# Kernel tuning notes

Hardware: AMD Instinct MI355X
Metric: run time of the kernel (lower is better)

Reference implementation:

```python
import jax, jax.numpy as jnp
import numpy as np
from jax import lax

# Dims: mel, reduction factor, encoder dim, prenet hidden, attention dim,
# attention-RNN units, decoder-RNN units, location-conv filters/kernel.
MEL, R, ENC, PRE, ATTN, ARNN, DRNN, FILT, K = 80, 2, 512, 256, 128, 1024, 1024, 32, 31
B, T_ENC, T_DEC = 64, 200, 400


def setup_inputs() -> dict:
    key = jax.random.key(0)
    ks = jax.random.split(key, 16)
    g = lambda i, shape: jax.random.normal(ks[i], shape, jnp.float32) * 0.02
    return {
        "encoder_outputs": jax.random.normal(ks[0], (B, T_ENC, ENC), jnp.float32),
        "inputs": jax.random.normal(ks[1], (B, T_DEC, MEL), jnp.float32),
        # prenet
        "W_pre1": g(2, (PRE, MEL)), "b_pre1": jnp.zeros((PRE,), jnp.float32),
        "W_pre2": g(3, (PRE, PRE)), "b_pre2": jnp.zeros((PRE,), jnp.float32),
        # memory layer (no bias)
        "W_mem": g(4, (ATTN, ENC)),
        # attention LSTMCell: input = prenet(256) + context(512)
        "Wih_a": g(5, (4 * ARNN, PRE + ENC)), "Whh_a": g(6, (4 * ARNN, ARNN)),
        "bih_a": jnp.zeros((4 * ARNN,), jnp.float32), "bhh_a": jnp.zeros((4 * ARNN,), jnp.float32),
        # location-sensitive attention
        "W_q": g(7, (ATTN, ARNN)),
        "W_conv": g(8, (FILT, 1, K)),
        "W_loc": g(9, (ATTN, FILT)),
        "v": g(10, (ATTN,)),
        # decoder LSTMCell: input = attn_rnn_h(1024) + context(512)
        "Wih_d": g(11, (4 * DRNN, ARNN + ENC)), "Whh_d": g(12, (4 * DRNN, DRNN)),
        "bih_d": jnp.zeros((4 * DRNN,), jnp.float32), "bhh_d": jnp.zeros((4 * DRNN,), jnp.float32),
        # output projections from cat(decoder_h, context) = 1536
        "W_mel": g(13, (MEL * R, DRNN + ENC)), "b_mel": jnp.zeros((MEL * R,), jnp.float32),
        "W_stop": g(14, (1, DRNN + ENC)), "b_stop": jnp.zeros((1,), jnp.float32),
    }


def _lstm(x, h, c, Wih, Whh, bih, bhh):
    # torch LSTMCell gate order: i, f, g, o
    gates = x @ Wih.T + bih + h @ Whh.T + bhh
    i, f, gg, o = jnp.split(gates, 4, axis=-1)
    c2 = jax.nn.sigmoid(f) * c + jax.nn.sigmoid(i) * jnp.tanh(gg)
    return jax.nn.sigmoid(o) * jnp.tanh(c2), c2


def _forward(encoder_outputs, inputs, W_pre1, b_pre1, W_pre2, b_pre2, W_mem,
             Wih_a, Whh_a, bih_a, bhh_a, W_q, W_conv, W_loc, v,
             Wih_d, Whh_d, bih_d, bhh_d, W_mel, b_mel, W_stop, b_stop):
    b, t_enc, _ = encoder_outputs.shape
    steps = inputs.shape[1] // R
    pm = encoder_outputs @ W_mem.T  # (B, T_enc, ATTN) processed memory
    # teacher-forced inputs: step 0 uses zeros, step k uses inputs[:, k*R-1]
    tf = inputs[:, R - 1::R, :][:, :steps - 1, :]
    dec_in = jnp.concatenate([jnp.zeros((b, 1, MEL), inputs.dtype), tf], axis=1).transpose(1, 0, 2)
    pad = (K - 1) // 2

    def step(carry, x):
        ah, ac, dh, dc, ctx, aw = carry
        # prenet (dropout disabled / eval mode)
        p = jax.nn.relu(jax.nn.relu(x @ W_pre1.T + b_pre1) @ W_pre2.T + b_pre2)
        ah, ac = _lstm(jnp.concatenate([p, ctx], -1), ah, ac, Wih_a, Whh_a, bih_a, bhh_a)
        # location feature from previous alignment: conv1d over time
        loc = lax.conv_general_dilated(aw[:, None, :], W_conv, (1,), [(pad, pad)],
                                       dimension_numbers=("NCH", "OIH", "NCH"))  # (B, FILT, T_enc)
        feat = jnp.tanh((ah @ W_q.T)[:, None, :] + jnp.einsum("bft,af->bta", loc, W_loc) + pm)
        align = jax.nn.softmax(jnp.einsum("bta,a->bt", feat, v), axis=-1)  # (B, T_enc)
        ctx = jnp.einsum("bt,btd->bd", align, encoder_outputs)  # (B, ENC)
        dh, dc = _lstm(jnp.concatenate([ah, ctx], -1), dh, dc, Wih_d, Whh_d, bih_d, bhh_d)
        proj = jnp.concatenate([dh, ctx], -1)  # (B, DRNN+ENC)
        mel = (proj @ W_mel.T + b_mel).reshape(b, R, MEL)
        stop = jax.nn.sigmoid(proj @ W_stop.T + b_stop)[:, 0]
        return (ah, ac, dh, dc, ctx, align), (mel, stop, align)

    z = lambda d: jnp.zeros((b, d), encoder_outputs.dtype)
    carry0 = (z(ARNN), z(ARNN), z(DRNN), z(DRNN), z(ENC),
              jnp.zeros((b, t_enc), encoder_outputs.dtype))
    _, (mels, stops, aligns) = lax.scan(step, carry0, dec_in)
    mel_outputs = mels.transpose(1, 0, 2, 3).reshape(b, steps * R, MEL)  # (B, T_dec, MEL)
    stop_tokens = jnp.repeat(stops.transpose(1, 0), R, axis=1)  # (B, T_dec)
    attn_scores = aligns.transpose(1, 0, 2)  # (B, steps, T_enc)
    return mel_outputs, stop_tokens, attn_scores


def reference(encoder_outputs, inputs, W_pre1, b_pre1, W_pre2, b_pre2, W_mem,
              Wih_a, Whh_a, bih_a, bhh_a, W_q, W_conv, W_loc, v,
              Wih_d, Whh_d, bih_d, bhh_d, W_mel, b_mel, W_stop, b_stop):
    return _forward(encoder_outputs, inputs, W_pre1, b_pre1, W_pre2, b_pre2, W_mem,
                    Wih_a, Whh_a, bih_a, bhh_a, W_q, W_conv, W_loc, v,
                    Wih_d, Whh_d, bih_d, bhh_d, W_mel, b_mel, W_stop, b_stop)
```

## Files before the change

### kernel.cpp

```cpp
#include <hip/hip_runtime.h>
#include <hip/hip_bf16.h>
#include <stdint.h>

#define STEPS  200
#define KA     1792
#define KD     2560
#define SLOT   (64*2560)

using bf16 = __bf16;
typedef __bf16 bf16x8 __attribute__((ext_vector_type(8)));
typedef float  f32x4  __attribute__((ext_vector_type(4)));
typedef unsigned int       u32;
typedef unsigned long long u64;

union U2h { u32 u; bf16 h[2]; };

#define MFMA16(a,b,c) __builtin_amdgcn_mfma_f32_16x16x32_bf16((a),(b),(c),0,0,0)

__device__ __forceinline__ float sigf(float x){ return 1.f/(1.f+__expf(-x)); }
__device__ __forceinline__ float tanhf_(float x){
  float ax = fabsf(x);
  float e  = __expf(-2.f*ax);
  float t  = (1.f-e)/(1.f+e);
  return x < 0.f ? -t : t;
}

__global__ void cvt_kernel(const float* __restrict__ s, bf16* __restrict__ d, int n){
  int i = blockIdx.x*256 + threadIdx.x;
  if (i < n) d[i] = (bf16)s[i];
}
__global__ void cvt_pad_kernel(const float* __restrict__ s, bf16* __restrict__ d,
                               int rows, int cin, int cout){
  int i = blockIdx.x*256 + threadIdx.x;
  if (i >= rows*cout) return;
  int r = i / cout, c = i % cout;
  d[i] = (bf16)(c < cin ? s[(size_t)r*cin + c] : 0.f);
}
__global__ void build_wa_pack(const float* __restrict__ Wiha, const float* __restrict__ Whha,
                              bf16* __restrict__ d){
  int i = blockIdx.x*256 + threadIdx.x;
  if (i >= 4096*1792) return;
  int r = i / 1792, k = i % 1792;
  int q2 = r >> 4, g = (r >> 2) & 3, j = r & 3;
  int orig = g*1024 + q2*4 + j;
  float v = (k < 768) ? Wiha[(size_t)orig*768 + k] : Whha[(size_t)orig*1024 + (k - 768)];
  d[i] = (bf16)v;
}
__global__ void build_wd_pack(const float* __restrict__ Wihd, const float* __restrict__ Whhd,
                              bf16* __restrict__ d){
  int i = blockIdx.x*256 + threadIdx.x;
  if (i >= 4096*2560) return;
  int r = i / 2560, k = i % 2560;
  int q2 = r >> 4, g = (r >> 2) & 3, j = r & 3;
  int orig = g*1024 + q2*4 + j;
  float v;
  if (k < 512)        v = Wihd[(size_t)orig*1536 + 1024 + k];
  else if (k < 1536)  v = Wihd[(size_t)orig*1536 + (k - 512)];
  else                v = Whhd[(size_t)orig*1024 + (k - 1536)];
  d[i] = (bf16)v;
}
__global__ void build_wmelcat(const float* __restrict__ Wmel, const float* __restrict__ Wstop,
                              bf16* __restrict__ d){
  int i = blockIdx.x*256 + threadIdx.x;
  if (i >= 176*1536) return;
  int r = i / 1536, c = i % 1536;
  float v = (r < 160) ? Wmel[(size_t)r*1536 + c] : (r == 160 ? Wstop[c] : 0.f);
  d[i] = (bf16)v;
}
__global__ void build_misc2(const float* biha, const float* bhha, float* biasa2,
                            const float* bihd, const float* bhhd, float* biasd2,
                            const float* bmel, const float* bstop, float* bias176,
                            const float* Wloc, float* wlocT){
  int i = blockIdx.x*256 + threadIdx.x;
  if (i < 4096){
    int q2 = i >> 4, g = (i >> 2) & 3, j = i & 3;
    int orig = g*1024 + q2*4 + j;
    biasa2[i] = biha[orig] + bhha[orig];
  } else if (i < 8192){
    int r = i - 4096;
    int q2 = r >> 4, g = (r >> 2) & 3, j = r & 3;
    int orig = g*1024 + q2*4 + j;
    biasd2[r] = bihd[orig] + bhhd[orig];
  } else if (i < 8192+176){
    int j = i - 8192;
    bias176[j] = (j < 160) ? bmel[j] : (j == 160 ? bstop[0] : 0.f);
  } else if (i < 8192+176+4096){
    int t = i - 8368;
    int f = t >> 7, a = t & 127;
    wlocT[t] = Wloc[a*32 + f];
  }
}
__global__ void build_decin(const float* __restrict__ inp, bf16* __restrict__ d){
  int i = blockIdx.x*256 + threadIdx.x;
  if (i >= 12800*96) return;
  int row = i / 96, c = i % 96;
  int s = row >> 6, b = row & 63;
  float v = 0.f;
  if (c < 80 && s > 0) v = inp[((size_t)b*400 + (2*s - 1))*80 + c];
  d[i] = (bf16)v;
}

template<int ACT, int OBF>
__global__ __launch_bounds__(256)
void gemm_k(const bf16* __restrict__ A, const bf16* __restrict__ Bm,
            const float* __restrict__ bias, float* __restrict__ Cf,
            bf16* __restrict__ Cb, int M, int N, int K, int MT)
{
  int wid = blockIdx.x*4 + (threadIdx.x >> 6);
  if (wid >= MT*(N >> 4)) return;
  int wm = wid % MT, wn = wid / MT;
  int l = threadIdx.x & 63, lo = l & 15, hi = l >> 4;
  const bf16* Bp = Bm + (size_t)(wn*16 + lo)*K + hi*8;
  const bf16* Ap = A  + (size_t)(wm*64 + lo)*K + hi*8;
  f32x4 acc0 = {0,0,0,0}, acc1 = {0,0,0,0}, acc2 = {0,0,0,0}, acc3 = {0,0,0,0};
  for (int k = 0; k < K; k += 32){
    bf16x8 bb = *(const bf16x8*)(Bp + k);
    bf16x8 a0 = *(const bf16x8*)(Ap + k);
    bf16x8 a1 = *(const bf16x8*)(Ap + (size_t)16*K + k);
    bf16x8 a2 = *(const bf16x8*)(Ap + (size_t)32*K + k);
    bf16x8 a3 = *(const bf16x8*)(Ap + (size_t)48*K + k);
    acc0 = MFMA16(a0, bb, acc0);
    acc1 = MFMA16(a1, bb, acc1);
    acc2 = MFMA16(a2, bb, acc2);
    acc3 = MFMA16(a3, bb, acc3);
  }
  int n = wn*16 + lo;
  float bv = bias ? bias[n] : 0.f;
  int m0 = wm*64 + hi*4;
  #pragma unroll
  for (int mt = 0; mt < 4; ++mt){
    f32x4 av = (mt==0)?acc0:(mt==1)?acc1:(mt==2)?acc2:acc3;
    #pragma unroll
    for (int r = 0; r < 4; ++r){
      float v = av[r] + bv;
      if (ACT) v = fmaxf(v, 0.f);
      size_t idx = (size_t)(m0 + mt*16 + r)*N + n;
      if (OBF) Cb[idx] = (bf16)v; else Cf[idx] = v;
    }
  }
}

__global__ __launch_bounds__(1024, 8)
void gates_step(const bf16* __restrict__ pall,
                const bf16* __restrict__ Wa, const bf16* __restrict__ Wd2,
                const float* __restrict__ biasa2, const float* __restrict__ biasd2,
                const bf16* __restrict__ slotPrev, bf16* __restrict__ slotCur,
                float* __restrict__ aC, float* __restrict__ dC,
                bf16* __restrict__ proj, int i, int doA, int doD)
{
  const bool isA = blockIdx.x < 256;
  if (isA ? !doA : !doD) return;
  const int tid = threadIdx.x;
  const int l = tid & 63, lo = l & 15, hi = l >> 4;
  const int wv = tid >> 6;
  const int kq = wv & 3;
  const int m0 = (wv >> 2) * 16;
  const int bq = isA ? blockIdx.x : blockIdx.x - 256;
  const int n0 = bq * 16;
  const int K  = isA ? KA : KD;
  const int JQ = isA ? 14 : 20;
  const bf16* Wg = isA ? Wa : Wd2;
  const float* bias2 = isA ? biasa2 : biasd2;
  float* Cst = (isA ? aC : dC) + (size_t)bq*64*4;

  __shared__ float red[4][64][17];

  const bf16* Wp0  = Wg + (size_t)(n0 + lo)*K + hi*8;
  const bf16* Xrow = slotPrev + (size_t)(m0 + lo)*2560 + hi*8;
  const bf16* Prow = pall + ((size_t)i*64 + m0 + lo)*256 + hi*8;
  const int kbase = kq * (K >> 2);
  f32x4 acc0 = {0,0,0,0};
  #pragma unroll 4
  for (int jj = 0; jj < JQ; ++jj){
    int k = kbase + jj*32;
    const bf16* ap;
    if (isA) ap = (k < 256) ? (Prow + k) : (Xrow + (k - 256));
    else     ap = Xrow + k;
    bf16x8 a  = *(const bf16x8*)ap;
    bf16x8 b0 = *(const bf16x8*)(Wp0 + k);
    acc0 = MFMA16(a, b0, acc0);
  }
  #pragma unroll
  for (int r = 0; r < 4; ++r)
    red[kq][m0 + hi*4 + r][lo] = acc0[r];
  __syncthreads();
  if (tid < 256){
    const int b  = tid >> 2;
    const int j4 = tid & 3;
    float gi = red[0][b][     j4] + red[1][b][     j4] + red[2][b][     j4] + red[3][b][     j4] + bias2[n0 +      j4];
    float gf = red[0][b][ 4 + j4] + red[1][b][ 4 + j4] + red[2][b][ 4 + j4] + red[3][b][ 4 + j4] + bias2[n0 +  4 + j4];
    float gg = red[0][b][ 8 + j4] + red[1][b][ 8 + j4] + red[2][b][ 8 + j4] + red[3][b][ 8 + j4] + bias2[n0 +  8 + j4];
    float go = red[0][b][12 + j4] + red[1][b][12 + j4] + red[2][b][12 + j4] + red[3][b][12 + j4] + bias2[n0 + 12 + j4];
    float* cp = Cst + b*4 + j4;
    float c = sigf(gf)*(*cp) + sigf(gi)*tanhf_(gg);
    float h = sigf(go)*tanhf_(c);
    *cp = c;
    bf16 hb = (bf16)h;
    const int u = bq*4 + j4;
    if (isA){
      slotCur[(size_t)b*2560 + 512 + u] = hb;
    } else {
      slotCur[(size_t)b*2560 + 1536 + u] = hb;
      proj[((size_t)(i-1)*64 + b)*1536 + u] = hb;
    }
  }
}

__global__ __launch_bounds__(1024)
void attn_step(const bf16* __restrict__ Wqb, const float* __restrict__ Wconv,
               const float* __restrict__ wlocTg, const float* __restrict__ vvp,
               const float* __restrict__ pm, const bf16* __restrict__ enc_bf,
               const float* __restrict__ alignPrev,
               bf16* __restrict__ slotCur, bf16* __restrict__ proj,
               float* __restrict__ out_attn, int i)
{
  const int tid = threadIdx.x;
  const int l = tid & 63, wv = tid >> 6;
  const int b = blockIdx.x;

  __shared__ __align__(16) bf16 ahs[1024];
  __shared__ float locb[200][32];
  __shared__ float awl[256];
  __shared__ float qp[1024];
  __shared__ float qv[128];
  __shared__ float es[200];
  __shared__ float sred[16];
  __shared__ float wlocT[32][128];
  __shared__ float credx[4][256];
  __shared__ float credy[4][256];

  if (tid < 256) awl[tid] = 0.f;
  if (i > 0 && tid < 200) awl[tid] = alignPrev[((size_t)b*200 + (i-1))*200 + tid];
  for (int it = tid; it < 4096; it += 1024)
    wlocT[it >> 7][it & 127] = wlocTg[it];
  if (tid < 128)
    *(bf16x8*)(&ahs[tid*8]) = *(const bf16x8*)(slotCur + (size_t)b*2560 + 512 + tid*8);
  __syncthreads();
  for (int it = tid; it < 6400; it += 1024){
    int f = it & 31, tl = it >> 5;
    float s = 0.f;
    #pragma unroll
    for (int j = 0; j < 31; ++j){
      int tt = tl + j - 15;
      if ((unsigned)tt < 200u) s += awl[tt]*Wconv[f*31+j];
    }
    locb[tl][f] = s;
  }
  {
    int a = tid & 127, seg = tid >> 7;
    const bf16* wr = Wqb + (size_t)a*1024 + seg*128;
    float s = 0.f;
    #pragma unroll
    for (int k2 = 0; k2 < 128; k2 += 8){
      bf16x8 x = *(const bf16x8*)(&ahs[seg*128 + k2]);
      bf16x8 y = *(const bf16x8*)(wr + k2);
      #pragma unroll
      for (int e = 0; e < 8; ++e) s += (float)x[e]*(float)y[e];
    }
    qp[tid] = s;
  }
  __syncthreads();
  if (tid < 128){
    float s = 0.f;
    #pragma unroll
    for (int sg = 0; sg < 8; ++sg) s += qp[tid + sg*128];
    qv[tid] = s;
  }
  __syncthreads();
  for (int tl = wv; tl < 200; tl += 16){
    const float* pmrow = pm + ((size_t)b*200 + tl)*128;
    const float* lrow  = locb[tl];
    float s = 0.f;
    #pragma unroll
    for (int half = 0; half < 2; ++half){
      int a = l + half*64;
      float x = qv[a] + pmrow[a];
      #pragma unroll
      for (int f = 0; f < 32; ++f) x += lrow[f]*wlocT[f][a];
      s += vvp[a]*tanhf_(x);
    }
    #pragma unroll
    for (int o = 32; o; o >>= 1) s += __shfl_xor(s, o);
    if (l == 0) es[tl] = s;
  }
  __syncthreads();
  {
    float e0 = (tid < 200) ? es[tid] : -3.0e38f;
    float m = e0;
    #pragma unroll
    for (int o = 32; o; o >>= 1) m = fmaxf(m, __shfl_xor(m, o));
    if (l == 0) sred[wv] = m;
    __syncthreads();
    m = fmaxf(fmaxf(sred[0],sred[1]), fmaxf(sred[2],sred[3]));
    float p = (tid < 200) ? __expf(e0 - m) : 0.f;
    float ss = p;
    #pragma unroll
    for (int o = 32; o; o >>= 1) ss += __shfl_xor(ss, o);
    __syncthreads();
    if (l == 0) sred[wv] = ss;
    __syncthreads();
    ss = sred[0]+sred[1]+sred[2]+sred[3];
    float aval = p / ss;
    if (tid < 200){
      awl[tid] = aval;
      out_attn[((size_t)b*200 + i)*200 + tid] = aval;
    }
  }
  __syncthreads();
  {
    const int col = tid & 255, tq = tid >> 8;
    const u32* ep = (const u32*)(enc_bf + (size_t)b*102400) + col;
    float x0 = 0.f, y0 = 0.f, x1 = 0.f, y1 = 0.f;
    const int t0 = tq*50;
    #pragma unroll 5
    for (int t = t0; t < t0 + 50; t += 2){
      U2h w0; w0.u = ep[(size_t)t*256];
      U2h w1; w1.u = ep[(size_t)(t+1)*256];
      float a0 = awl[t], a1 = awl[t+1];
      x0 += a0*(float)w0.h[0]; y0 += a0*(float)w0.h[1];
      x1 += a1*(float)w1.h[0]; y1 += a1*(float)w1.h[1];
    }
    credx[tq][col] = x0 + x1;
    credy[tq][col] = y0 + y1;
  }
  __syncthreads();
  if (tid < 256){
    float sx = credx[0][tid]+credx[1][tid]+credx[2][tid]+credx[3][tid];
    float sy = credy[0][tid]+credy[1][tid]+credy[2][tid]+credy[3][tid];
    U2h cb; cb.h[0] = (bf16)sx; cb.h[1] = (bf16)sy;
    *((u32*)(slotCur + (size_t)b*2560) + tid) = cb.u;
    *((u32*)(proj + ((size_t)i*64 + b)*1536 + 1024) + tid) = cb.u;
  }
}

__global__ void scatter_out(const float* __restrict__ mt_, float* __restrict__ out){
  int i = blockIdx.x*256 + threadIdx.x;
  const int NMEL = 12800*160;
  if (i < NMEL){
    int sb = i / 160, j = i % 160;
    int s = sb >> 6, b = sb & 63;
    int r = j / 80, mm = j % 80;
    out[((size_t)b*400 + 2*s + r)*80 + mm] = mt_[(size_t)sb*176 + j];
  } else if (i < NMEL + 12800){
    int sb = i - NMEL;
    int s = sb >> 6, b = sb & 63;
    float st = sigf(mt_[(size_t)sb*176 + 160]);
    float* so = out + 2048000;
    so[(size_t)b*400 + 2*s]     = st;
    so[(size_t)b*400 + 2*s + 1] = st;
  }
}

extern "C" void kernel_launch(void* const* d_in, const int* in_sizes, int n_in,
                              void* d_out, int out_size, void* d_ws, size_t ws_size,
                              hipStream_t stream)
{
  const float* enc   = (const float*)d_in[0];
  const float* inp   = (const float*)d_in[1];
  const float* Wpre1 = (const float*)d_in[2];
  const float* bpre1 = (const float*)d_in[3];
  const float* Wpre2 = (const float*)d_in[4];
  const float* bpre2 = (const float*)d_in[5];
  const float* Wmem  = (const float*)d_in[6];
  const float* Wiha  = (const float*)d_in[7];
  const float* Whha  = (const float*)d_in[8];
  const float* biha  = (const float*)d_in[9];
  const float* bhha  = (const float*)d_in[10];
  const float* Wq    = (const float*)d_in[11];
  const float* Wconv = (const float*)d_in[12];
  const float* Wloc  = (const float*)d_in[13];
  const float* vv    = (const float*)d_in[14];
  const float* Wihd  = (const float*)d_in[15];
  const float* Whhd  = (const float*)d_in[16];
  const float* bihd  = (const float*)d_in[17];
  const float* bhhd  = (const float*)d_in[18];
  const float* Wmel  = (const float*)d_in[19];
  const float* bmel  = (const float*)d_in[20];
  const float* Wstop = (const float*)d_in[21];
  const float* bstop = (const float*)d_in[22];
  float* out = (float*)d_out;

  char* pp = (char*)d_ws;
  auto carve = [&](size_t bytes)->char*{
    char* r = (char*)(((uintptr_t)pp + 255) & ~(uintptr_t)255);
    pp = r + bytes;
    return r;
  };
  bf16*  enc_bf  = (bf16*) carve((size_t)64*200*512*2);
  float* pm      = (float*)carve((size_t)64*200*128*4);
  bf16*  decin   = (bf16*) carve((size_t)12800*96*2);
  bf16*  h1      = (bf16*) carve((size_t)12800*256*2);
  bf16*  pall    = (bf16*) carve((size_t)12800*256*2);
  bf16*  Wp1b    = (bf16*) carve((size_t)256*96*2);
  bf16*  Wp2b    = (bf16*) carve((size_t)256*256*2);
  bf16*  Wmemb   = (bf16*) carve((size_t)128*512*2);
  bf16*  Wqb     = (bf16*) carve((size_t)128*1024*2);
  bf16*  Wca     = (bf16*) carve((size_t)4096*KA*2);
  bf16*  Wcd2    = (bf16*) carve((size_t)4096*KD*2);
  bf16*  Wmc     = (bf16*) carve((size_t)176*1536*2);
  float* biasa2  = (float*)carve(4096*4);
  float* biasd2  = (float*)carve(4096*4);
  float* bias176 = (float*)carve(176*4);
  float* wlocTg  = (float*)carve(4096*4);
  bf16*  proj    = (bf16*) carve((size_t)12800*1536*2);
  float* meltmp  = (float*)carve((size_t)12800*176*4);
  float* aC  = (float*)carve((size_t)256*64*4*4);
  float* dC  = (float*)carve((size_t)256*64*4*4);
  size_t zbytes = (size_t)((char*)dC + (size_t)256*64*4*4 - (char*)aC);
  bf16*  ring = (bf16*)carve((size_t)202*SLOT*2);
  hipMemsetAsync(aC, 0, zbytes, stream);
  hipMemsetAsync(ring, 0, (size_t)2*SLOT*2, stream);

  cvt_kernel<<<(6553600+255)/256,256,0,stream>>>(enc,   enc_bf, 6553600);
  cvt_kernel<<<(131072+255)/256, 256,0,stream>>>(Wq,    Wqb,    131072);
  cvt_kernel<<<(65536+255)/256,  256,0,stream>>>(Wmem,  Wmemb,  65536);
  cvt_kernel<<<(65536+255)/256,  256,0,stream>>>(Wpre2, Wp2b,   65536);
  cvt_pad_kernel<<<(256*96+255)/256,256,0,stream>>>(Wpre1, Wp1b, 256, 80, 96);
  build_wa_pack<<<(4096*1792+255)/256,256,0,stream>>>(Wiha, Whha, Wca);
  build_wd_pack<<<(4096*2560+255)/256,256,0,stream>>>(Wihd, Whhd, Wcd2);
  build_wmelcat<<<(176*1536+255)/256,256,0,stream>>>(Wmel, Wstop, Wmc);
  build_misc2<<<(8368+4096+255)/256,256,0,stream>>>(biha,bhha,biasa2, bihd,bhhd,biasd2,
                                                    bmel,bstop,bias176, Wloc, wlocTg);
  build_decin<<<(12800*96+255)/256,256,0,stream>>>(inp, decin);

  gemm_k<1,1><<<800,256,0,stream>>>(decin, Wp1b, bpre1, nullptr, h1, 12800,256,96, 200);
  gemm_k<1,1><<<800,256,0,stream>>>(h1, Wp2b, bpre2, nullptr, pall, 12800,256,256, 200);
  gemm_k<0,0><<<400,256,0,stream>>>(enc_bf, Wmemb, nullptr, pm, nullptr, 12800,128,512, 200);

  float* out_attn = out + 2073600;
  for (int i = 0; i <= STEPS; ++i){
    const bf16* slotPrev = ring + (size_t)i*SLOT;
    bf16*       slotCur  = ring + (size_t)(i+1)*SLOT;
    gates_step<<<512,1024,0,stream>>>(pall, Wca, Wcd2, biasa2, biasd2,
                                      slotPrev, slotCur, aC, dC, proj,
                                      i, i < STEPS ? 1 : 0, i > 0 ? 1 : 0);
    if (i < STEPS)
      attn_step<<<64,1024,0,stream>>>(Wqb, Wconv, wlocTg, vv, pm, enc_bf,
                                      out_attn, slotCur, proj, out_attn, i);
  }

  gemm_k<0,0><<<550,256,0,stream>>>(proj, Wmc, bias176, meltmp, nullptr, 12800,176,1536, 200);
  scatter_out<<<(12800*160+12800+255)/256,256,0,stream>>>(meltmp, out);
}
```

Before: 20.11 ms.

## Fuse per-step decoder kernels into one persistent kernel with grid barriers

Replaces the roughly 400 per-step kernel launches (gates_step plus attn_step) with a single persistent decoder_scan kernel of 256 blocks. Blocks synchronise through a hierarchical atomic grid barrier. The attention and decoder LSTM weight slices stay resident in LDS across all steps, with the decoder weights only partly cached and the rest read from global memory. Each block now computes both its attention-LSTM and decoder-LSTM gate slice, 64 blocks also run the attention for one batch row, and the previous alignment is kept in LDS instead of being reloaded. The change removes launch overhead and repeated weight fetches, but it depends on all 256 blocks being co-resident, since otherwise the barrier deadlocks. It also halves the number of parallel blocks per gate GEMM compared with the 512-block launch.

```diff
diff --git a/kernel.cpp b/kernel.cpp
--- a/kernel.cpp
+++ b/kernel.cpp
@@ -5,7 +5,17 @@
 #define STEPS  200
 #define KA     1792
 #define KD     2560
+#define NBLK   256
 #define SLOT   (64*2560)
+#define RELBASE 256
+#define JDA    56
+#define JDT    80
+#define JDL_ATTN 42
+#define OFF_WD   57344
+#define OFF_AWL  100352
+#define OFF_OVL  101376
+#define OFF_REDG 139264
+#define DSMEM  159744
 
 using bf16 = __bf16;
 typedef __bf16 bf16x8 __attribute__((ext_vector_type(8)));
@@ -23,6 +33,17 @@
   float e  = __expf(-2.f*ax);
   float t  = (1.f-e)/(1.f+e);
   return x < 0.f ? -t : t;
+}
+
+__device__ __forceinline__ u32 atom_peek(u32* p){
+  u32 old;
+  asm volatile("global_atomic_add %0, %1, %2, off sc0 sc1\n\t"
+               "s_waitcnt vmcnt(0)"
+               : "=v"(old) : "v"(p), "v"(0u) : "memory");
+  return old;
+}
+__device__ __forceinline__ void stu(u32* p, u32 v){
+  __hip_atomic_store(p, v, __ATOMIC_RELAXED, __HIP_MEMORY_SCOPE_AGENT);
 }
 
 __global__ void cvt_kernel(const float* __restrict__ s, bf16* __restrict__ d, int n){
@@ -140,196 +161,264 @@
   }
 }
 
-__global__ __launch_bounds__(1024, 8)
-void gates_step(const bf16* __restrict__ pall,
-                const bf16* __restrict__ Wa, const bf16* __restrict__ Wd2,
-                const float* __restrict__ biasa2, const float* __restrict__ biasd2,
-                const bf16* __restrict__ slotPrev, bf16* __restrict__ slotCur,
-                float* __restrict__ aC, float* __restrict__ dC,
-                bf16* __restrict__ proj, int i, int doA, int doD)
+__device__ __forceinline__ void gridbar(unsigned* cnt, unsigned nb){
+  __syncthreads();
+  const int tid = threadIdx.x;
+  if (tid == 0)
+    __hip_atomic_fetch_add(&cnt[(blockIdx.x >> 5)*16], 1u, __ATOMIC_RELAXED,
+                           __HIP_MEMORY_SCOPE_AGENT);
+  if (blockIdx.x == 0){
+    if (tid < 64){
+      const unsigned tgt = nb*32u;
+      for (;;){
+        bool ok = true;
+        if (tid < 8) ok = (atom_peek(&cnt[tid*16]) >= tgt);
+        if (__all(ok)) break;
+        __builtin_amdgcn_s_sleep(2);
+      }
+      __hip_atomic_fetch_add(&cnt[RELBASE + tid*16], 1u, __ATOMIC_RELAXED,
+                             __HIP_MEMORY_SCOPE_AGENT);
+    }
+  } else if (tid == 0){
+    u32* rl = &cnt[RELBASE + (blockIdx.x & 63u)*16];
+    while (atom_peek(rl) < nb)
+      __builtin_amdgcn_s_sleep(2);
+  }
+  __syncthreads();
+}
+
+__global__ __launch_bounds__(1024)
+void decoder_scan(const bf16* __restrict__ pall,
+                  const bf16* __restrict__ Wa, const bf16* __restrict__ Wd2,
+                  const float* __restrict__ biasa2, const float* __restrict__ biasd2,
+                  const bf16* __restrict__ Wqb, const float* __restrict__ Wconv,
+                  const float* __restrict__ wlocTg, const float* __restrict__ vvp,
+                  const float* __restrict__ pm, const bf16* __restrict__ enc_bf,
+                  bf16* __restrict__ ring,
+                  float* __restrict__ aC, float* __restrict__ dC,
+                  bf16* __restrict__ proj, float* __restrict__ out_attn,
+                  unsigned* __restrict__ cnt)
 {
-  const bool isA = blockIdx.x < 256;
-  if (isA ? !doA : !doD) return;
+  extern __shared__ char smem[];
   const int tid = threadIdx.x;
   const int l = tid & 63, lo = l & 15, hi = l >> 4;
   const int wv = tid >> 6;
-  const int kq = wv & 3;
-  const int m0 = (wv >> 2) * 16;
-  const int bq = isA ? blockIdx.x : blockIdx.x - 256;
+  const int kq = wv & 3, mg = wv >> 2;
+  const int m0 = mg * 16;
+  const int bq = blockIdx.x;
   const int n0 = bq * 16;
-  const int K  = isA ? KA : KD;
-  const int JQ = isA ? 14 : 20;
-  const bf16* Wg = isA ? Wa : Wd2;
-  const float* bias2 = isA ? biasa2 : biasd2;
-  float* Cst = (isA ? aC : dC) + (size_t)bq*64*4;
-
-  __shared__ float red[4][64][17];
-
-  const bf16* Wp0  = Wg + (size_t)(n0 + lo)*K + hi*8;
-  const bf16* Xrow = slotPrev + (size_t)(m0 + lo)*2560 + hi*8;
-  const bf16* Prow = pall + ((size_t)i*64 + m0 + lo)*256 + hi*8;
-  const int kbase = kq * (K >> 2);
-  f32x4 acc0 = {0,0,0,0};
-  #pragma unroll 4
-  for (int jj = 0; jj < JQ; ++jj){
-    int k = kbase + jj*32;
-    const bf16* ap;
-    if (isA) ap = (k < 256) ? (Prow + k) : (Xrow + (k - 256));
-    else     ap = Xrow + k;
-    bf16x8 a  = *(const bf16x8*)ap;
-    bf16x8 b0 = *(const bf16x8*)(Wp0 + k);
-    acc0 = MFMA16(a, b0, acc0);
-  }
-  #pragma unroll
-  for (int r = 0; r < 4; ++r)
-    red[kq][m0 + hi*4 + r][lo] = acc0[r];
+  const bool isAttn = blockIdx.x < 64;
+  const int JDL = isAttn ? JDL_ATTN : JDT;
+
+  bf16* wldsA = (bf16*)smem;
+  bf16* wldsD = (bf16*)(smem + OFF_WD);
+  float* awl  = (float*)(smem + OFF_AWL);
+  char*  ovl  = smem + OFF_OVL;
+  float* red  = isAttn ? (float*)ovl : (float*)(smem + OFF_REDG);
+  bf16*  ahs   = (bf16*)ovl;
+  float* locb  = (float*)(ovl + 2048);
+  float* qp    = (float*)(ovl + 27648);
+  float* qv    = (float*)(ovl + 31744);
+  float* es    = (float*)(ovl + 32256);
+  float* sredp = (float*)(ovl + 33280);
+  float* wlocT = (float*)(ovl + 33344);
+  float* credx = (float*)(ovl + 49728);
+  float* credy = (float*)(ovl + 53824);
+
+  for (int j = wv; j < JDA; j += 16)
+    *(bf16x8*)(wldsA + ((size_t)(j*64 + l))*8) =
+      *(const bf16x8*)(Wa + (size_t)(n0 + lo)*KA + j*32 + hi*8);
+  for (int j = wv; j < JDL; j += 16)
+    *(bf16x8*)(wldsD + ((size_t)(j*64 + l))*8) =
+      *(const bf16x8*)(Wd2 + (size_t)(n0 + lo)*KD + j*32 + hi*8);
+  if (isAttn){
+    if (tid < 256) awl[tid] = 0.f;
+    for (int it = tid; it < 4096; it += 1024) wlocT[it] = wlocTg[it];
+  }
   __syncthreads();
-  if (tid < 256){
-    const int b  = tid >> 2;
-    const int j4 = tid & 3;
-    float gi = red[0][b][     j4] + red[1][b][     j4] + red[2][b][     j4] + red[3][b][     j4] + bias2[n0 +      j4];
-    float gf = red[0][b][ 4 + j4] + red[1][b][ 4 + j4] + red[2][b][ 4 + j4] + red[3][b][ 4 + j4] + bias2[n0 +  4 + j4];
-    float gg = red[0][b][ 8 + j4] + red[1][b][ 8 + j4] + red[2][b][ 8 + j4] + red[3][b][ 8 + j4] + bias2[n0 +  8 + j4];
-    float go = red[0][b][12 + j4] + red[1][b][12 + j4] + red[2][b][12 + j4] + red[3][b][12 + j4] + bias2[n0 + 12 + j4];
-    float* cp = Cst + b*4 + j4;
-    float c = sigf(gf)*(*cp) + sigf(gi)*tanhf_(gg);
-    float h = sigf(go)*tanhf_(c);
-    *cp = c;
-    bf16 hb = (bf16)h;
-    const int u = bq*4 + j4;
-    if (isA){
-      slotCur[(size_t)b*2560 + 512 + u] = hb;
-    } else {
-      slotCur[(size_t)b*2560 + 1536 + u] = hb;
-      proj[((size_t)(i-1)*64 + b)*1536 + u] = hb;
+  unsigned nb = 0;
+  gridbar(cnt, ++nb);
+
+  for (int i = 0; i <= STEPS; ++i){
+    const bf16* slotPrev = ring + (size_t)i*SLOT;
+    bf16*       slotCur  = ring + (size_t)(i+1)*SLOT;
+    const bf16* Xrow = slotPrev + (size_t)(m0 + lo)*2560 + hi*8;
+
+    if (i < STEPS){
+      const bf16* Prow = pall + ((size_t)i*64 + m0 + lo)*256 + hi*8;
+      f32x4 acc = {0,0,0,0};
+      #pragma unroll
+      for (int jj = 0; jj < 14; ++jj){
+        int j = kq*14 + jj, k = j*32;
+        const bf16* ap = (k < 256) ? (Prow + k) : (Xrow + (k - 256));
+        bf16x8 a = *(const bf16x8*)ap;
+        bf16x8 b = *(const bf16x8*)(wldsA + ((size_t)(j*64 + l))*8);
+        acc = MFMA16(a, b, acc);
+      }
+      #pragma unroll
+      for (int r = 0; r < 4; ++r)
+        red[((size_t)kq*64 + m0 + hi*4 + r)*17 + lo] = acc[r];
+      __syncthreads();
+      if (tid < 128){
+        const int b = tid >> 1, jp = (tid & 1)*2;
+        U2h hp;
+        #pragma unroll
+        for (int t = 0; t < 2; ++t){
+          int j4 = jp + t;
+          float gi = red[(0*64+b)*17+     j4] + red[(1*64+b)*17+     j4] + red[(2*64+b)*17+     j4] + red[(3*64+b)*17+     j4] + biasa2[n0 +      j4];
+          float gf = red[(0*64+b)*17+ 4 + j4] + red[(1*64+b)*17+ 4 + j4] + red[(2*64+b)*17+ 4 + j4] + red[(3*64+b)*17+ 4 + j4] + biasa2[n0 +  4 + j4];
+          float gg = red[(0*64+b)*17+ 8 + j4] + red[(1*64+b)*17+ 8 + j4] + red[(2*64+b)*17+ 8 + j4] + red[(3*64+b)*17+ 8 + j4] + biasa2[n0 +  8 + j4];
+          float go = red[(0*64+b)*17+12 + j4] + red[(1*64+b)*17+12 + j4] + red[(2*64+b)*17+12 + j4] + red[(3*64+b)*17+12 + j4] + biasa2[n0 + 12 + j4];
+          float* cp = aC + (size_t)bq*256 + b*4 + j4;
+          float c = sigf(gf)*(*cp) + sigf(gi)*tanhf_(gg);
+          float h = sigf(go)*tanhf_(c);
+          *cp = c;
+          hp.h[t] = (bf16)h;
+        }
+        stu((u32*)(slotCur + (size_t)b*2560 + 512 + bq*4 + jp), hp.u);
+      }
+      __syncthreads();
     }
-  }
-}
-
-__global__ __launch_bounds__(1024)
-void attn_step(const bf16* __restrict__ Wqb, const float* __restrict__ Wconv,
-               const float* __restrict__ wlocTg, const float* __restrict__ vvp,
-               const float* __restrict__ pm, const bf16* __restrict__ enc_bf,
-               const float* __restrict__ alignPrev,
-               bf16* __restrict__ slotCur, bf16* __restrict__ proj,
-               float* __restrict__ out_attn, int i)
-{
-  const int tid = threadIdx.x;
-  const int l = tid & 63, wv = tid >> 6;
-  const int b = blockIdx.x;
-
-  __shared__ __align__(16) bf16 ahs[1024];
-  __shared__ float locb[200][32];
-  __shared__ float awl[256];
-  __shared__ float qp[1024];
-  __shared__ float qv[128];
-  __shared__ float es[200];
-  __shared__ float sred[16];
-  __shared__ float wlocT[32][128];
-  __shared__ float credx[4][256];
-  __shared__ float credy[4][256];
-
-  if (tid < 256) awl[tid] = 0.f;
-  if (i > 0 && tid < 200) awl[tid] = alignPrev[((size_t)b*200 + (i-1))*200 + tid];
-  for (int it = tid; it < 4096; it += 1024)
-    wlocT[it >> 7][it & 127] = wlocTg[it];
-  if (tid < 128)
-    *(bf16x8*)(&ahs[tid*8]) = *(const bf16x8*)(slotCur + (size_t)b*2560 + 512 + tid*8);
-  __syncthreads();
-  for (int it = tid; it < 6400; it += 1024){
-    int f = it & 31, tl = it >> 5;
-    float s = 0.f;
-    #pragma unroll
-    for (int j = 0; j < 31; ++j){
-      int tt = tl + j - 15;
-      if ((unsigned)tt < 200u) s += awl[tt]*Wconv[f*31+j];
+    if (i > 0){
+      f32x4 acc = {0,0,0,0};
+      #pragma unroll
+      for (int jj = 0; jj < 20; ++jj){
+        int j = kq*20 + jj, k = j*32;
+        bf16x8 a = *(const bf16x8*)(Xrow + k);
+        bf16x8 b;
+        if (j < JDL) b = *(const bf16x8*)(wldsD + ((size_t)(j*64 + l))*8);
+        else         b = *(const bf16x8*)(Wd2 + (size_t)(n0 + lo)*KD + k + hi*8);
+        acc = MFMA16(a, b, acc);
+      }
+      #pragma unroll
+      for (int r = 0; r < 4; ++r)
+        red[((size_t)kq*64 + m0 + hi*4 + r)*17 + lo] = acc[r];
+      __syncthreads();
+      if (tid < 128){
+        const int b = tid >> 1, jp = (tid & 1)*2;
+        U2h hp;
+        #pragma unroll
+        for (int t = 0; t < 2; ++t){
+          int j4 = jp + t;
+          float gi = red[(0*64+b)*17+     j4] + red[(1*64+b)*17+     j4] + red[(2*64+b)*17+     j4] + red[(3*64+b)*17+     j4] + biasd2[n0 +      j4];
+          float gf = red[(0*64+b)*17+ 4 + j4] + red[(1*64+b)*17+ 4 + j4] + red[(2*64+b)*17+ 4 + j4] + red[(3*64+b)*17+ 4 + j4] + biasd2[n0 +  4 + j4];
+          float gg = red[(0*64+b)*17+ 8 + j4] + red[(1*64+b)*17+ 8 + j4] + red[(2*64+b)*17+ 8 + j4] + red[(3*64+b)*17+ 8 + j4] + biasd2[n0 +  8 + j4];
+          float go = red[(0*64+b)*17+12 + j4] + red[(1*64+b)*17+12 + j4] + red[(2*64+b)*17+12 + j4] + red[(3*64+b)*17+12 + j4] + biasd2[n0 + 12 + j4];
+          float* cp = dC + (size_t)bq*256 + b*4 + j4;
+          float c = sigf(gf)*(*cp) + sigf(gi)*tanhf_(gg);
+          float h = sigf(go)*tanhf_(c);
+          *cp = c;
+          hp.h[t] = (bf16)h;
+        }
+        stu((u32*)(slotCur + (size_t)b*2560 + 1536 + bq*4 + jp), hp.u);
+        *(u32*)(proj + ((size_t)(i-1)*64 + b)*1536 + bq*4 + jp) = hp.u;
+      }
     }
-    locb[tl][f] = s;
-  }
-  {
-    int a = tid & 127, seg = tid >> 7;
-    const bf16* wr = Wqb + (size_t)a*1024 + seg*128;
-    float s = 0.f;
-    #pragma unroll
-    for (int k2 = 0; k2 < 128; k2 += 8){
-      bf16x8 x = *(const bf16x8*)(&ahs[seg*128 + k2]);
-      bf16x8 y = *(const bf16x8*)(wr + k2);
-      #pragma unroll
-      for (int e = 0; e < 8; ++e) s += (float)x[e]*(float)y[e];
+    gridbar(cnt, ++nb);
+
+    if (isAttn && i < STEPS){
+      const int b = blockIdx.x;
+      if (tid < 128)
+        *(bf16x8*)(&ahs[tid*8]) = *(const bf16x8*)(slotCur + (size_t)b*2560 + 512 + tid*8);
+      __syncthreads();
+      for (int it = tid; it < 6400; it += 1024){
+        int f = it & 31, tl = it >> 5;
+        float s = 0.f;
+        #pragma unroll
+        for (int j = 0; j < 31; ++j){
+          int tt = tl + j - 15;
+          if ((unsigned)tt < 200u) s += awl[tt]*Wconv[f*31+j];
+        }
+        locb[tl*32 + f] = s;
+      }
+      {
+        int a = tid & 127, seg = tid >> 7;
+        const bf16* wr = Wqb + (size_t)a*1024 + seg*128;
+        float s = 0.f;
+        #pragma unroll
+        for (int k2 = 0; k2 < 128; k2 += 8){
+          bf16x8 x = *(const bf16x8*)(&ahs[seg*128 + k2]);
+          bf16x8 y = *(const bf16x8*)(wr + k2);
+          #pragma unroll
+          for (int e = 0; e < 8; ++e) s += (float)x[e]*(float)y[e];
+        }
+        qp[tid] = s;
+      }
+      __syncthreads();
+      if (tid < 128){
+        float s = 0.f;
+        #pragma unroll
+        for (int sg = 0; sg < 8; ++sg) s += qp[tid + sg*128];
+        qv[tid] = s;
+      }
+      __syncthreads();
+      for (int tl = wv; tl < 200; tl += 16){
+        const float* pmrow = pm + ((size_t)b*200 + tl)*128;
+        const float* lrow  = locb + tl*32;
+        float s = 0.f;
+        #pragma unroll
+        for (int half = 0; half < 2; ++half){
+          int a = l + half*64;
+          float x = qv[a] + pmrow[a];
+          #pragma unroll
+          for (int f = 0; f < 32; ++f) x += lrow[f]*wlocT[f*128 + a];
+          s += vvp[a]*tanhf_(x);
+        }
+        #pragma unroll
+        for (int o = 32; o; o >>= 1) s += __shfl_xor(s, o);
+        if (l == 0) es[tl] = s;
+      }
+      __syncthreads();
+      {
+        float e0 = (tid < 200) ? es[tid] : -3.0e38f;
+        float m = e0;
+        #pragma unroll
+        for (int o = 32; o; o >>= 1) m = fmaxf(m, __shfl_xor(m, o));
+        if (l == 0) sredp[wv] = m;
+        __syncthreads();
+        m = fmaxf(fmaxf(sredp[0],sredp[1]), fmaxf(sredp[2],sredp[3]));
+        float p = (tid < 200) ? __expf(e0 - m) : 0.f;
+        float ss = p;
+        #pragma unroll
+        for (int o = 32; o; o >>= 1) ss += __shfl_xor(ss, o);
+        __syncthreads();
+        if (l == 0) sredp[wv] = ss;
+        __syncthreads();
+        ss = sredp[0]+sredp[1]+sredp[2]+sredp[3];
+        float aval = p / ss;
+        if (tid < 256) {
+          float nv = (tid < 200) ? aval : 0.f;
+          awl[tid] = nv;
+        }
+        if (tid < 200) out_attn[((size_t)b*200 + i)*200 + tid] = aval;
+      }
+      __syncthreads();
+      {
+        const int col = tid & 255, tq = tid >> 8;
+        const u32* ep = (const u32*)(enc_bf + (size_t)b*102400) + col;
+        float x0 = 0.f, y0 = 0.f, x1 = 0.f, y1 = 0.f;
+        const int t0 = tq*50;
+        #pragma unroll 5
+        for (int t = t0; t < t0 + 50; t += 2){
+          U2h w0; w0.u = ep[(size_t)t*256];
+          U2h w1; w1.u = ep[(size_t)(t+1)*256];
+          float a0 = awl[t], a1 = awl[t+1];
+          x0 += a0*(float)w0.h[0]; y0 += a0*(float)w0.h[1];
+          x1 += a1*(float)w1.h[0]; y1 += a1*(float)w1.h[1];
+        }
+        credx[tq*256 + col] = x0 + x1;
+        credy[tq*256 + col] = y0 + y1;
+      }
+      __syncthreads();
+      if (tid < 256){
+        float sx = credx[tid]+credx[256+tid]+credx[512+tid]+credx[768+tid];
+        float sy = credy[tid]+credy[256+tid]+credy[512+tid]+credy[768+tid];
+        U2h cb; cb.h[0] = (bf16)sx; cb.h[1] = (bf16)sy;
+        stu((u32*)(slotCur + (size_t)b*2560) + tid, cb.u);
+        *((u32*)(proj + ((size_t)i*64 + b)*1536 + 1024) + tid) = cb.u;
+      }
     }
-    qp[tid] = s;
-  }
-  __syncthreads();
-  if (tid < 128){
-    float s = 0.f;
-    #pragma unroll
-    for (int sg = 0; sg < 8; ++sg) s += qp[tid + sg*128];
-    qv[tid] = s;
-  }
-  __syncthreads();
-  for (int tl = wv; tl < 200; tl += 16){
-    const float* pmrow = pm + ((size_t)b*200 + tl)*128;
-    const float* lrow  = locb[tl];
-    float s = 0.f;
-    #pragma unroll
-    for (int half = 0; half < 2; ++half){
-      int a = l + half*64;
-      float x = qv[a] + pmrow[a];
-      #pragma unroll
-      for (int f = 0; f < 32; ++f) x += lrow[f]*wlocT[f][a];
-      s += vvp[a]*tanhf_(x);
-    }
-    #pragma unroll
-    for (int o = 32; o; o >>= 1) s += __shfl_xor(s, o);
-    if (l == 0) es[tl] = s;
-  }
-  __syncthreads();
-  {
-    float e0 = (tid < 200) ? es[tid] : -3.0e38f;
-    float m = e0;
-    #pragma unroll
-    for (int o = 32; o; o >>= 1) m = fmaxf(m, __shfl_xor(m, o));
-    if (l == 0) sred[wv] = m;
-    __syncthreads();
-    m = fmaxf(fmaxf(sred[0],sred[1]), fmaxf(sred[2],sred[3]));
-    float p = (tid < 200) ? __expf(e0 - m) : 0.f;
-    float ss = p;
-    #pragma unroll
-    for (int o = 32; o; o >>= 1) ss += __shfl_xor(ss, o);
-    __syncthreads();
-    if (l == 0) sred[wv] = ss;
-    __syncthreads();
-    ss = sred[0]+sred[1]+sred[2]+sred[3];
-    float aval = p / ss;
-    if (tid < 200){
-      awl[tid] = aval;
-      out_attn[((size_t)b*200 + i)*200 + tid] = aval;
-    }
-  }
-  __syncthreads();
-  {
-    const int col = tid & 255, tq = tid >> 8;
-    const u32* ep = (const u32*)(enc_bf + (size_t)b*102400) + col;
-    float x0 = 0.f, y0 = 0.f, x1 = 0.f, y1 = 0.f;
-    const int t0 = tq*50;
-    #pragma unroll 5
-    for (int t = t0; t < t0 + 50; t += 2){
-      U2h w0; w0.u = ep[(size_t)t*256];
-      U2h w1; w1.u = ep[(size_t)(t+1)*256];
-      float a0 = awl[t], a1 = awl[t+1];
-      x0 += a0*(float)w0.h[0]; y0 += a0*(float)w0.h[1];
-      x1 += a1*(float)w1.h[0]; y1 += a1*(float)w1.h[1];
-    }
-    credx[tq][col] = x0 + x1;
-    credy[tq][col] = y0 + y1;
-  }
-  __syncthreads();
-  if (tid < 256){
-    float sx = credx[0][tid]+credx[1][tid]+credx[2][tid]+credx[3][tid];
-    float sy = credy[0][tid]+credy[1][tid]+credy[2][tid]+credy[3][tid];
-    U2h cb; cb.h[0] = (bf16)sx; cb.h[1] = (bf16)sy;
-    *((u32*)(slotCur + (size_t)b*2560) + tid) = cb.u;
-    *((u32*)(proj + ((size_t)i*64 + b)*1536 + 1024) + tid) = cb.u;
+    gridbar(cnt, ++nb);
   }
 }
 
@@ -406,7 +495,8 @@
   float* meltmp  = (float*)carve((size_t)12800*176*4);
   float* aC  = (float*)carve((size_t)256*64*4*4);
   float* dC  = (float*)carve((size_t)256*64*4*4);
-  size_t zbytes = (size_t)((char*)dC + (size_t)256*64*4*4 - (char*)aC);
+  unsigned* cnt = (unsigned*)carve(16384);
+  size_t zbytes = (size_t)((char*)cnt + 16384 - (char*)aC);
   bf16*  ring = (bf16*)carve((size_t)202*SLOT*2);
   hipMemsetAsync(aC, 0, zbytes, stream);
   hipMemsetAsync(ring, 0, (size_t)2*SLOT*2, stream);
@@ -427,17 +517,12 @@
   gemm_k<1,1><<<800,256,0,stream>>>(h1, Wp2b, bpre2, nullptr, pall, 12800,256,256, 200);
   gemm_k<0,0><<<400,256,0,stream>>>(enc_bf, Wmemb, nullptr, pm, nullptr, 12800,128,512, 200);
 
+  hipFuncSetAttribute((const void*)decoder_scan,
+                      hipFuncAttributeMaxDynamicSharedMemorySize, DSMEM);
   float* out_attn = out + 2073600;
-  for (int i = 0; i <= STEPS; ++i){
-    const bf16* slotPrev = ring + (size_t)i*SLOT;
-    bf16*       slotCur  = ring + (size_t)(i+1)*SLOT;
-    gates_step<<<512,1024,0,stream>>>(pall, Wca, Wcd2, biasa2, biasd2,
-                                      slotPrev, slotCur, aC, dC, proj,
-                                      i, i < STEPS ? 1 : 0, i > 0 ? 1 : 0);
-    if (i < STEPS)
-      attn_step<<<64,1024,0,stream>>>(Wqb, Wconv, wlocTg, vv, pm, enc_bf,
-                                      out_attn, slotCur, proj, out_attn, i);
-  }
+  decoder_scan<<<NBLK,1024,DSMEM,stream>>>(pall, Wca, Wcd2, biasa2, biasd2,
+                                           Wqb, Wconv, wlocTg, vv, pm, enc_bf,
+                                           ring, aC, dC, proj, out_attn, cnt);
 
   gemm_k<0,0><<<550,256,0,stream>>>(proj, Wmc, bias176, meltmp, nullptr, 12800,176,1536, 200);
   scatter_out<<<(12800*160+12800+255)/256,256,0,stream>>>(meltmp, out);
```

Result: slower. 27.79 ms (+38.2%).
